# Performance work log

Measured on AMD Instinct MI355X. Metric: run time of the kernel, lower is better.

Reference implementation:

```python
import jax, jax.numpy as jnp
import numpy as np

MULT = 0.0025
EPS = 1e-6  # torch F.pairwise_distance eps added to the difference


def setup_inputs() -> dict:
    key = jax.random.key(0)
    k1, k2, k3, k4 = jax.random.split(key, 4)
    B, K, N = 256, 51, 8192
    y_hat = jax.random.uniform(k1, (B, K), dtype=jnp.float32)
    y = jax.random.uniform(k2, (B, K), dtype=jnp.float32)
    face = jax.random.normal(k3, (N, 3), dtype=jnp.float32)
    bs_tensor = jax.random.normal(k4, (K, N, 3), dtype=jnp.float32)
    return {"y_hat": y_hat, "y": y, "face": face, "bs_tensor": bs_tensor}


def _reconstruct(w, face, bs_tensor):
    # face: [N,3], bs_tensor: [K,N,3], w: [B,K] -> [B,N,3]
    # Contract over blendshape dim directly (avoids the [B,K,N,3] intermediate).
    return face[None] + jnp.einsum('bk,knd->bnd', w, bs_tensor)


def reference(y_hat, y, face, bs_tensor):
    yh_face = _reconstruct(y_hat, face, bs_tensor)  # [B,N,3]
    y_face = _reconstruct(y, face, bs_tensor)       # [B,N,3]
    # transpose(1,2) -> [B,3,N]; pairwise_distance norms over last dim (N)
    diff = jnp.swapaxes(yh_face, 1, 2) - jnp.swapaxes(y_face, 1, 2) + EPS
    dist = jnp.sqrt(jnp.sum(diff * diff, axis=-1))  # [B,3]
    return jnp.sum(dist) * MULT
```

## Files before the change

### kernel.cpp

```cpp
#include <hip/hip_runtime.h>
#include <math.h>

#define NPTS     8192
#define KDIM     51
#define KPAD     64
#define CHUNKS   64
#define CHUNK_N  128
#define MULT     0.0025f

typedef short short8  __attribute__((ext_vector_type(8)));
typedef float float4v __attribute__((ext_vector_type(4)));
typedef float float4a __attribute__((ext_vector_type(4), aligned(4)));

__device__ __forceinline__ unsigned short f32_to_bf16(float f) {
    unsigned int u = __float_as_uint(f);
    unsigned int r = u + 0x7FFFu + ((u >> 16) & 1u);
    return (unsigned short)(r >> 16);
}

__global__ __launch_bounds__(256) void pl_gram(
    const float* __restrict__ bs, float* __restrict__ partial,
    float* __restrict__ pq, unsigned int* __restrict__ ctr) {
  __shared__ unsigned short lds16[KPAD * 136];

  const int bx  = blockIdx.x;
  const int tid = threadIdx.x;

  if (bx == 192) {
    for (int i = tid; i < 768; i += 256) pq[i] = 0.0f;
    if (tid == 0) ctr[0] = 0u;
    return;
  }

  const int d   = bx / CHUNKS;
  const int n0  = (bx % CHUNKS) * CHUNK_N;

  unsigned int* lds32 = (unsigned int*)lds16;
  for (int u = tid; u < KPAD * (CHUNK_N / 2); u += 256) {
    int np = u & 63;
    int k  = u >> 6;
    float v0 = 0.0f, v1 = 0.0f;
    if (k < KDIM) {
      const float* p = bs + (size_t)k * (NPTS * 3) + (size_t)(n0 + 2 * np) * 3 + d;
      float4a f = *(const float4a*)p;
      v0 = f[0];
      v1 = f[3];
    }
    lds32[k * 68 + np] = (unsigned int)f32_to_bf16(v0) |
                         ((unsigned int)f32_to_bf16(v1) << 16);
  }
  __syncthreads();

  const int wave  = tid >> 6;
  const int lane  = tid & 63;
  const int m16   = lane & 15;
  const int quad  = lane >> 4;
  const int rbase = (wave >> 1) * 32;
  const int cbase = (wave & 1) * 32;

  float4v acc00 = {0.f, 0.f, 0.f, 0.f}, acc01 = {0.f, 0.f, 0.f, 0.f};
  float4v acc10 = {0.f, 0.f, 0.f, 0.f}, acc11 = {0.f, 0.f, 0.f, 0.f};

#pragma unroll
  for (int p0 = 0; p0 < CHUNK_N; p0 += 32) {
    const int po = p0 + quad * 8;
    short8 a0 = *(const short8*)&lds16[(rbase +      m16) * 136 + po];
    short8 a1 = *(const short8*)&lds16[(rbase + 16 + m16) * 136 + po];
    short8 b0 = *(const short8*)&lds16[(cbase +      m16) * 136 + po];
    short8 b1 = *(const short8*)&lds16[(cbase + 16 + m16) * 136 + po];
    acc00 = __builtin_amdgcn_mfma_f32_16x16x32_bf16(a0, b0, acc00, 0, 0, 0);
    acc01 = __builtin_amdgcn_mfma_f32_16x16x32_bf16(a0, b1, acc01, 0, 0, 0);
    acc10 = __builtin_amdgcn_mfma_f32_16x16x32_bf16(a1, b0, acc10, 0, 0, 0);
    acc11 = __builtin_amdgcn_mfma_f32_16x16x32_bf16(a1, b1, acc11, 0, 0, 0);
  }

  float* pout = partial + (size_t)bx * 4096;
#pragma unroll
  for (int r = 0; r < 4; ++r) {
    int row0 = rbase + quad * 4 + r;
    int col0 = cbase + m16;
    pout[row0 * 64 + col0]               = acc00[r];
    pout[row0 * 64 + (col0 + 16)]        = acc01[r];
    pout[(row0 + 16) * 64 + col0]        = acc10[r];
    pout[(row0 + 16) * 64 + (col0 + 16)] = acc11[r];
  }
}

__global__ __launch_bounds__(256) void pl_finalize(
    const float* __restrict__ partial, float* __restrict__ pq,
    unsigned int* __restrict__ ctr, const float* __restrict__ yh,
    const float* __restrict__ yv, float* __restrict__ out) {
  __shared__ __align__(16) float Gl[256];
  __shared__ __align__(16) float wl[64 * 68];
  __shared__ unsigned int lflag;
  __shared__ float redw[4];

  const int bx  = blockIdx.x;
  const int d   = bx / 52;
  const int rem = bx - d * 52;
  const int rg  = rem >> 2;
  const int b0  = (rem & 3) * 64;
  const int tid = threadIdx.x;

  {
    const float* p = partial + (size_t)(d * CHUNKS) * 4096 + rg * 256 + tid;
    float s = 0.0f;
#pragma unroll 16
    for (int c = 0; c < CHUNKS; ++c) s += p[(size_t)c * 4096];
    Gl[tid] = s;
  }

  for (int i = tid; i < 64 * KDIM; i += 256) {
    int bl = i / KDIM, k = i - bl * KDIM;
    int gi = (b0 + bl) * KDIM + k;
    wl[bl * 68 + k] = yh[gi] - yv[gi];
  }
  for (int i = tid; i < 64 * 13; i += 256) {
    int bl = i / 13, c = KDIM + (i - bl * 13);
    wl[bl * 68 + c] = 0.0f;
  }
  __syncthreads();

  {
    const int jt = tid & 15;
    const int bh = tid >> 4;
    float4v g4[4];
#pragma unroll
    for (int ri = 0; ri < 4; ++ri)
      g4[ri] = *(const float4v*)&Gl[ri * 64 + jt * 4];

#pragma unroll
    for (int bl = 0; bl < 4; ++bl) {
      const int lb = bl * 16 + bh;
      float4v wj = *(const float4v*)&wl[lb * 68 + jt * 4];
      float4v wk = *(const float4v*)&wl[lb * 68 + rg * 4];
      float pqp = 0.0f;
#pragma unroll
      for (int ri = 0; ri < 4; ++ri) {
        float t = 0.0f;
#pragma unroll
        for (int jj = 0; jj < 4; ++jj) t = fmaf(g4[ri][jj], wj[jj], t);
        pqp = fmaf(wk[ri], t, pqp);
      }
#pragma unroll
      for (int off = 1; off < 16; off <<= 1) pqp += __shfl_xor(pqp, off, 16);
      if (jt == 0) atomicAdd(&pq[d * 256 + b0 + lb], pqp);
    }
  }
  __syncthreads();

  if (tid == 0) {
    unsigned int old = __hip_atomic_fetch_add(ctr, 1u, __ATOMIC_RELEASE,
                                              __HIP_MEMORY_SCOPE_AGENT);
    lflag = (old == 155u) ? 1u : 0u;
  }
  __syncthreads();
  if (lflag == 0u) return;

  if (tid == 0)
    (void)__hip_atomic_load(ctr, __ATOMIC_ACQUIRE, __HIP_MEMORY_SCOPE_AGENT);
  __syncthreads();

  float s = 0.0f;
#pragma unroll
  for (int i = 0; i < 3; ++i) {
    float q = __hip_atomic_load(&pq[i * 256 + tid], __ATOMIC_RELAXED,
                                __HIP_MEMORY_SCOPE_AGENT);
    s += sqrtf(q);
  }
  for (int off = 32; off; off >>= 1) s += __shfl_down(s, off, 64);
  if ((tid & 63) == 0) redw[tid >> 6] = s;
  __syncthreads();
  if (tid == 0)
    out[0] = (redw[0] + redw[1] + redw[2] + redw[3]) * MULT;
}

extern "C" void kernel_launch(void* const* d_in, const int* in_sizes, int n_in,
                              void* d_out, int out_size, void* d_ws, size_t ws_size,
                              hipStream_t stream) {
  const float* y_hat = (const float*)d_in[0];
  const float* y     = (const float*)d_in[1];
  const float* bs    = (const float*)d_in[3];
  float* out = (float*)d_out;

  float* partial    = (float*)d_ws;
  float* pq         = partial + (size_t)3 * CHUNKS * 4096;
  unsigned int* ctr = (unsigned int*)(pq + 768);

  pl_gram<<<3 * CHUNKS + 1, 256, 0, stream>>>(bs, partial, pq, ctr);
  pl_finalize<<<156, 256, 0, stream>>>(partial, pq, ctr, y_hat, y, out);
}
```

Measured before the change: 19.64 us.

## Fuse gram and finalize kernels with a spin-wait counter barrier

Merges the gram-partial and finalize stages into one launch. The finalize blocks preload their weight differences, then spin on a global counter until all gram blocks have published their partials. A small init kernel now does the zeroing separately, so the launch count stays at two. This is meant to overlap finalize setup with gram compute and hide the inter-kernel gap, but it relies on all 348 blocks being co-resident to avoid deadlock, and the spinning adds polling traffic.

```diff
diff --git a/kernel.cpp b/kernel.cpp
--- a/kernel.cpp
+++ b/kernel.cpp
@@ -7,6 +7,9 @@
 #define CHUNKS   64
 #define CHUNK_N  128
 #define MULT     0.0025f
+#define GBLK     192
+#define FBLK     156
+#define TBLK     (GBLK + FBLK)
 
 typedef short short8  __attribute__((ext_vector_type(8)));
 typedef float float4v __attribute__((ext_vector_type(4)));
@@ -18,106 +21,121 @@
     return (unsigned short)(r >> 16);
 }
 
-__global__ __launch_bounds__(256) void pl_gram(
+__global__ __launch_bounds__(256) void pl_init(float* __restrict__ pq,
+                                               unsigned int* __restrict__ ctr) {
+  const int tid = threadIdx.x;
+  pq[tid] = 0.0f; pq[256 + tid] = 0.0f; pq[512 + tid] = 0.0f;
+  if (tid == 0) ctr[0] = 0u;
+}
+
+__global__ __launch_bounds__(256) void pl_fused(
     const float* __restrict__ bs, float* __restrict__ partial,
-    float* __restrict__ pq, unsigned int* __restrict__ ctr) {
-  __shared__ unsigned short lds16[KPAD * 136];
+    float* __restrict__ pq, unsigned int* __restrict__ ctr,
+    const float* __restrict__ yh, const float* __restrict__ yv,
+    float* __restrict__ out) {
+  __shared__ __align__(16) char smem[18448];
+  __shared__ unsigned int lflag;
+  __shared__ float redw[4];
 
   const int bx  = blockIdx.x;
   const int tid = threadIdx.x;
 
-  if (bx == 192) {
-    for (int i = tid; i < 768; i += 256) pq[i] = 0.0f;
-    if (tid == 0) ctr[0] = 0u;
+  if (bx < GBLK) {
+    unsigned short* lds16 = (unsigned short*)smem;
+    const int d  = bx / CHUNKS;
+    const int n0 = (bx % CHUNKS) * CHUNK_N;
+
+    unsigned int* lds32 = (unsigned int*)lds16;
+    for (int u = tid; u < KPAD * (CHUNK_N / 2); u += 256) {
+      int np = u & 63;
+      int k  = u >> 6;
+      float v0 = 0.0f, v1 = 0.0f;
+      if (k < KDIM) {
+        const float* p = bs + (size_t)k * (NPTS * 3) + (size_t)(n0 + 2 * np) * 3 + d;
+        float4a f = *(const float4a*)p;
+        v0 = f[0];
+        v1 = f[3];
+      }
+      lds32[k * 68 + np] = (unsigned int)f32_to_bf16(v0) |
+                           ((unsigned int)f32_to_bf16(v1) << 16);
+    }
+    __syncthreads();
+
+    const int wave  = tid >> 6;
+    const int lane  = tid & 63;
+    const int m16   = lane & 15;
+    const int quad  = lane >> 4;
+    const int rbase = (wave >> 1) * 32;
+    const int cbase = (wave & 1) * 32;
+
+    float4v acc00 = {0.f, 0.f, 0.f, 0.f}, acc01 = {0.f, 0.f, 0.f, 0.f};
+    float4v acc10 = {0.f, 0.f, 0.f, 0.f}, acc11 = {0.f, 0.f, 0.f, 0.f};
+
+#pragma unroll
+    for (int p0 = 0; p0 < CHUNK_N; p0 += 32) {
+      const int po = p0 + quad * 8;
+      short8 a0 = *(const short8*)&lds16[(rbase +      m16) * 136 + po];
+      short8 a1 = *(const short8*)&lds16[(rbase + 16 + m16) * 136 + po];
+      short8 b0 = *(const short8*)&lds16[(cbase +      m16) * 136 + po];
+      short8 b1 = *(const short8*)&lds16[(cbase + 16 + m16) * 136 + po];
+      acc00 = __builtin_amdgcn_mfma_f32_16x16x32_bf16(a0, b0, acc00, 0, 0, 0);
+      acc01 = __builtin_amdgcn_mfma_f32_16x16x32_bf16(a0, b1, acc01, 0, 0, 0);
+      acc10 = __builtin_amdgcn_mfma_f32_16x16x32_bf16(a1, b0, acc10, 0, 0, 0);
+      acc11 = __builtin_amdgcn_mfma_f32_16x16x32_bf16(a1, b1, acc11, 0, 0, 0);
+    }
+
+    float* pout = partial + (size_t)bx * 4096;
+#pragma unroll
+    for (int r = 0; r < 4; ++r) {
+      int row0 = rbase + quad * 4 + r;
+      int col0 = cbase + m16;
+      pout[row0 * 64 + col0]               = acc00[r];
+      pout[row0 * 64 + (col0 + 16)]        = acc01[r];
+      pout[(row0 + 16) * 64 + col0]        = acc10[r];
+      pout[(row0 + 16) * 64 + (col0 + 16)] = acc11[r];
+    }
+
+    __syncthreads();
+    if (tid == 0)
+      __hip_atomic_fetch_add(ctr, 1u, __ATOMIC_RELEASE,
+                             __HIP_MEMORY_SCOPE_AGENT);
     return;
   }
 
-  const int d   = bx / CHUNKS;
-  const int n0  = (bx % CHUNKS) * CHUNK_N;
-
-  unsigned int* lds32 = (unsigned int*)lds16;
-  for (int u = tid; u < KPAD * (CHUNK_N / 2); u += 256) {
-    int np = u & 63;
-    int k  = u >> 6;
-    float v0 = 0.0f, v1 = 0.0f;
-    if (k < KDIM) {
-      const float* p = bs + (size_t)k * (NPTS * 3) + (size_t)(n0 + 2 * np) * 3 + d;
-      float4a f = *(const float4a*)p;
-      v0 = f[0];
-      v1 = f[3];
-    }
-    lds32[k * 68 + np] = (unsigned int)f32_to_bf16(v0) |
-                         ((unsigned int)f32_to_bf16(v1) << 16);
-  }
-  __syncthreads();
-
-  const int wave  = tid >> 6;
-  const int lane  = tid & 63;
-  const int m16   = lane & 15;
-  const int quad  = lane >> 4;
-  const int rbase = (wave >> 1) * 32;
-  const int cbase = (wave & 1) * 32;
-
-  float4v acc00 = {0.f, 0.f, 0.f, 0.f}, acc01 = {0.f, 0.f, 0.f, 0.f};
-  float4v acc10 = {0.f, 0.f, 0.f, 0.f}, acc11 = {0.f, 0.f, 0.f, 0.f};
-
-#pragma unroll
-  for (int p0 = 0; p0 < CHUNK_N; p0 += 32) {
-    const int po = p0 + quad * 8;
-    short8 a0 = *(const short8*)&lds16[(rbase +      m16) * 136 + po];
-    short8 a1 = *(const short8*)&lds16[(rbase + 16 + m16) * 136 + po];
-    short8 b0 = *(const short8*)&lds16[(cbase +      m16) * 136 + po];
-    short8 b1 = *(const short8*)&lds16[(cbase + 16 + m16) * 136 + po];
-    acc00 = __builtin_amdgcn_mfma_f32_16x16x32_bf16(a0, b0, acc00, 0, 0, 0);
-    acc01 = __builtin_amdgcn_mfma_f32_16x16x32_bf16(a0, b1, acc01, 0, 0, 0);
-    acc10 = __builtin_amdgcn_mfma_f32_16x16x32_bf16(a1, b0, acc10, 0, 0, 0);
-    acc11 = __builtin_amdgcn_mfma_f32_16x16x32_bf16(a1, b1, acc11, 0, 0, 0);
-  }
-
-  float* pout = partial + (size_t)bx * 4096;
-#pragma unroll
-  for (int r = 0; r < 4; ++r) {
-    int row0 = rbase + quad * 4 + r;
-    int col0 = cbase + m16;
-    pout[row0 * 64 + col0]               = acc00[r];
-    pout[row0 * 64 + (col0 + 16)]        = acc01[r];
-    pout[(row0 + 16) * 64 + col0]        = acc10[r];
-    pout[(row0 + 16) * 64 + (col0 + 16)] = acc11[r];
-  }
-}
-
-__global__ __launch_bounds__(256) void pl_finalize(
-    const float* __restrict__ partial, float* __restrict__ pq,
-    unsigned int* __restrict__ ctr, const float* __restrict__ yh,
-    const float* __restrict__ yv, float* __restrict__ out) {
-  __shared__ __align__(16) float Gl[256];
-  __shared__ __align__(16) float wl[64 * 68];
-  __shared__ unsigned int lflag;
-  __shared__ float redw[4];
-
-  const int bx  = blockIdx.x;
-  const int d   = bx / 52;
-  const int rem = bx - d * 52;
+  float* Gl = (float*)smem;
+  float* wl = (float*)(smem + 1024);
+
+  const int fx  = bx - GBLK;
+  const int d   = fx / 52;
+  const int rem = fx - d * 52;
   const int rg  = rem >> 2;
   const int b0  = (rem & 3) * 64;
-  const int tid = threadIdx.x;
+
+  for (int i = tid; i < 64 * KDIM; i += 256) {
+    int bl = i / KDIM, k = i - bl * KDIM;
+    int gi = (b0 + bl) * KDIM + k;
+    wl[bl * 68 + k] = yh[gi] - yv[gi];
+  }
+  for (int i = tid; i < 64 * 13; i += 256) {
+    int bl = i / 13, c = KDIM + (i - bl * 13);
+    wl[bl * 68 + c] = 0.0f;
+  }
+
+  if (tid == 0) {
+    while (__hip_atomic_load(ctr, __ATOMIC_RELAXED,
+                             __HIP_MEMORY_SCOPE_AGENT) < (unsigned)GBLK)
+      __builtin_amdgcn_s_sleep(8);
+  }
+  __syncthreads();
 
   {
     const float* p = partial + (size_t)(d * CHUNKS) * 4096 + rg * 256 + tid;
     float s = 0.0f;
 #pragma unroll 16
-    for (int c = 0; c < CHUNKS; ++c) s += p[(size_t)c * 4096];
+    for (int c = 0; c < CHUNKS; ++c)
+      s += __hip_atomic_load(&p[(size_t)c * 4096], __ATOMIC_RELAXED,
+                             __HIP_MEMORY_SCOPE_AGENT);
     Gl[tid] = s;
-  }
-
-  for (int i = tid; i < 64 * KDIM; i += 256) {
-    int bl = i / KDIM, k = i - bl * KDIM;
-    int gi = (b0 + bl) * KDIM + k;
-    wl[bl * 68 + k] = yh[gi] - yv[gi];
-  }
-  for (int i = tid; i < 64 * 13; i += 256) {
-    int bl = i / 13, c = KDIM + (i - bl * 13);
-    wl[bl * 68 + c] = 0.0f;
   }
   __syncthreads();
 
@@ -152,7 +170,7 @@
   if (tid == 0) {
     unsigned int old = __hip_atomic_fetch_add(ctr, 1u, __ATOMIC_RELEASE,
                                               __HIP_MEMORY_SCOPE_AGENT);
-    lflag = (old == 155u) ? 1u : 0u;
+    lflag = (old == (TBLK - 1)) ? 1u : 0u;
   }
   __syncthreads();
   if (lflag == 0u) return;
@@ -187,6 +205,6 @@
   float* pq         = partial + (size_t)3 * CHUNKS * 4096;
   unsigned int* ctr = (unsigned int*)(pq + 768);
 
-  pl_gram<<<3 * CHUNKS + 1, 256, 0, stream>>>(bs, partial, pq, ctr);
-  pl_finalize<<<156, 256, 0, stream>>>(partial, pq, ctr, y_hat, y, out);
-}
+  pl_init<<<1, 256, 0, stream>>>(pq, ctr);
+  pl_fused<<<TBLK, 256, 0, stream>>>(bs, partial, pq, ctr, y_hat, y, out);
+}
```

Result: slower. 37.52 us (+91.1%).
